# Kernel optimization log

Hardware: AMD Instinct MI355X
Metric: run time of the kernel (lower is better)

Reference implementation:

```python
import jax, jax.numpy as jnp
import numpy as np

DIM = 512; NB = 4; BS = DIM // NB            # EinFFT blocks
DS = 64; DC = 4; EXP = 2; DI = EXP * DIM      # Mamba dims
DTR = DIM // 16                               # dt_rank
BLOCKS = 2; LAM = 0.01; B_SZ = 2; L_SZ = 1024

def layer_norm(x, w, b):
    m = x.mean(-1, keepdims=True)
    v = x.var(-1, keepdims=True)
    return (x - m) / jnp.sqrt(v + 1e-5) * w + b

def softshrink(x, lam):
    return jnp.where(x > lam, x - lam, jnp.where(x < -lam, x + lam, jnp.zeros((), x.dtype)))

def mamba(x, in_proj_w, conv_w, conv_b, x_proj_w, dt_proj_w, dt_proj_b, A_log, D, out_proj_w):
    B, L, _ = x.shape
    xz = x @ in_proj_w.T                      # (B,L,2*DI)
    xm, z = jnp.split(xz, 2, axis=-1)
    # causal depthwise conv1d, keep first L outputs
    xt = xm.transpose(0, 2, 1)                # (B,DI,L)
    conv = jax.lax.conv_general_dilated(xt, conv_w, (1,), [(DC - 1, 0)],
                                        feature_group_count=DI,
                                        dimension_numbers=('NCH', 'OIH', 'NCH'))
    xm = jax.nn.silu((conv + conv_b[None, :, None]).transpose(0, 2, 1))  # (B,L,DI)
    proj = xm @ x_proj_w.T                    # (B,L,DTR+2*DS)
    dt = proj[..., :DTR]
    Bm = proj[..., DTR:DTR + DS]
    Cm = proj[..., DTR + DS:]
    dt = jax.nn.softplus(dt @ dt_proj_w.T + dt_proj_b)   # (B,L,DI)
    A = -jnp.exp(A_log)                       # (DI,DS)

    def step(h, inp):
        dt_t, B_t, C_t, u_t = inp             # (B,DI),(B,DS),(B,DS),(B,DI)
        dA = jnp.exp(dt_t[:, :, None] * A)
        h = dA * h + dt_t[:, :, None] * B_t[:, None, :] * u_t[:, :, None]
        y = jnp.einsum('bds,bs->bd', h, C_t)
        return h, y

    h0 = jnp.zeros((B, DI, DS), x.dtype)
    _, ys = jax.lax.scan(step, h0, (dt.transpose(1, 0, 2), Bm.transpose(1, 0, 2),
                                    Cm.transpose(1, 0, 2), xm.transpose(1, 0, 2)))
    y = ys.transpose(1, 0, 2) + xm * D        # (B,L,DI)
    y = y * jax.nn.silu(z)
    return y @ out_proj_w.T

def einfft(x, cw1, cw2, cb1, cb2):
    B, N, C = x.shape
    xf = jnp.fft.fft2(x.reshape(B, N, NB, BS), axes=(1, 2), norm='ortho')
    mul = lambda t, w: jnp.einsum('BNbd,bdk->BNbk', t, w)
    r1 = jax.nn.relu(mul(xf.real, cw1[0]) - mul(xf.imag, cw1[1]) + cb1[0])
    i1 = jax.nn.relu(mul(xf.real, cw1[1]) + mul(xf.imag, cw1[0]) + cb1[1])
    r2 = softshrink(mul(r1, cw2[0]) - mul(i1, cw2[1]) + cb2[0], LAM)
    i2 = softshrink(mul(r1, cw2[1]) + mul(i1, cw2[0]) + cb2[1], LAM)
    out = jnp.fft.ifft2(r2 + 1j * i2, axes=(1, 2), norm='ortho')
    return out.real.astype(x.dtype).reshape(B, N, C)

def setup_inputs() -> dict:
    key = jax.random.key(0)
    ks = jax.random.split(key, 16)
    r = lambda i, shape, s: jax.random.normal(ks[i], shape, jnp.float32) * s
    A_log = jnp.log(jnp.tile(jnp.arange(1, DS + 1, dtype=jnp.float32), (DI, 1)))
    return {
        'x': jax.random.normal(ks[0], (B_SZ, L_SZ, DIM), jnp.float32),
        'ln_w': jnp.ones((DIM,), jnp.float32), 'ln_b': jnp.zeros((DIM,), jnp.float32),
        'in_proj_w': r(1, (2 * DI, DIM), 0.02),
        'conv_w': r(2, (DI, 1, DC), 0.1), 'conv_b': jnp.zeros((DI,), jnp.float32),
        'x_proj_w': r(3, (DTR + 2 * DS, DI), 0.02),
        'dt_proj_w': r(4, (DI, DTR), 0.02),
        'dt_proj_b': jnp.full((DI,), float(np.log(np.expm1(0.01))), jnp.float32),
        'A_log': A_log, 'D': jnp.ones((DI,), jnp.float32),
        'out_proj_w': r(5, (DIM, DI), 0.02),
        'norm2_w': jnp.ones((DIM,), jnp.float32), 'norm2_b': jnp.zeros((DIM,), jnp.float32),
        'cw1': r(6, (2, NB, BS, BS), 0.02), 'cw2': r(7, (2, NB, BS, BS), 0.02),
        'cb1': r(8, (2, NB, BS), 0.02), 'cb2': r(9, (2, NB, BS), 0.02),
    }

def reference(x, ln_w, ln_b, in_proj_w, conv_w, conv_b, x_proj_w, dt_proj_w, dt_proj_b,
              A_log, D, out_proj_w, norm2_w, norm2_b, cw1, cw2, cb1, cb2):
    for _ in range(BLOCKS):
        x = x + mamba(layer_norm(x, ln_w, ln_b), in_proj_w, conv_w, conv_b,
                      x_proj_w, dt_proj_w, dt_proj_b, A_log, D, out_proj_w)
        x = x + einfft(layer_norm(x, norm2_w, norm2_b), cw1, cw2, cb1, cb2)
    return x
```

## Files before the change

### kernel.cpp

```cpp
#include <hip/hip_runtime.h>

typedef unsigned short u16;
typedef __attribute__((ext_vector_type(8))) short bf8;
typedef __attribute__((ext_vector_type(4))) float f4;

__device__ __forceinline__ float bf2f(u16 b) {
    return __uint_as_float(((unsigned)b) << 16);
}
__device__ __forceinline__ u16 f2bf(float f) {
    unsigned u = __float_as_uint(f);
    u += 0x7fffu + ((u >> 16) & 1u);
    return (u16)(u >> 16);
}
__device__ __forceinline__ void pack8f(const float* v, u16* dst) {
    uint r0 = (uint)f2bf(v[0]) | ((uint)f2bf(v[1]) << 16);
    uint r1 = (uint)f2bf(v[2]) | ((uint)f2bf(v[3]) << 16);
    uint r2 = (uint)f2bf(v[4]) | ((uint)f2bf(v[5]) << 16);
    uint r3 = (uint)f2bf(v[6]) | ((uint)f2bf(v[7]) << 16);
    *(uint4*)dst = make_uint4(r0, r1, r2, r3);
}
__device__ __forceinline__ bf8 neg8(bf8 v) {
    union { bf8 b; uint u[4]; } t; t.b = v;
    t.u[0] ^= 0x80008000u; t.u[1] ^= 0x80008000u;
    t.u[2] ^= 0x80008000u; t.u[3] ^= 0x80008000u;
// ... 106 lines not shown
}

#define LSTR 40
template <int TAF, int EPI>
__global__ __launch_bounds__(256)
void mgemm_k(const void* __restrict__ Ap, const u16* __restrict__ Bp,
             float* __restrict__ D, int N, int K, int lda, int ldb, int ldc,
             long bsA, long bsB, long bsC,
             const float* __restrict__ bias, const float* __restrict__ res) {
    const float* Af = (const float*)Ap + blockIdx.z * bsA;
    const u16*  Ab  = (const u16*)Ap + blockIdx.z * bsA;
    const u16*  B   = Bp + blockIdx.z * bsB;
    D += blockIdx.z * bsC;

    __shared__ u16 As[64 * LSTR];
    __shared__ u16 Bs[64 * LSTR];
    const int tid = threadIdx.x;
    const int lane = tid & 63;
    const int w = tid >> 6, wm = w & 1, wn = w >> 1;
    const int m0 = blockIdx.y * 64, n0 = blockIdx.x * 64;
    const int fr = (lane & 15), fq = (lane >> 4);

    f4 acc[2][2] = {};

    for (int k0 = 0; k0 < K; k0 += 32) {
        {
            const int ar = tid >> 2, aks = (tid & 3) << 3;
            if constexpr (TAF == 1) {
                *(uint4*)&As[ar * LSTR + aks] =
                    *(const uint4*)(Ab + (long)(m0 + ar) * lda + k0 + aks);
            } else if constexpr (TAF == 2) {
                const float* p = Af + (long)(m0 + ar) * lda + k0 + aks;
                float4 x = *(const float4*)p, y = *(const float4*)(p + 4);
#pragma unroll
                for (int pt = 1; pt < 4; ++pt) {
                    const float* pp = p + (long)pt * bsA;
                    float4 x1 = *(const float4*)pp, y1 = *(const float4*)(pp + 4);
                    x.x += x1.x; x.y += x1.y; x.z += x1.z; x.w += x1.w;
                    y.x += y1.x; y.y += y1.y; y.z += y1.z; y.w += y1.w;
                }
                float tv[8];
                tv[0] = x.x; tv[1] = x.y; tv[2] = x.z; tv[3] = x.w;
                tv[4] = y.x; tv[5] = y.y; tv[6] = y.z; tv[7] = y.w;
                pack8f(tv, &As[ar * LSTR + aks]);
            } else {
                const float* p = Af + (long)(m0 + ar) * lda + k0 + aks;
                float tv[8];
                float4 x = *(const float4*)p, y = *(const float4*)(p + 4);
                tv[0] = x.x; tv[1] = x.y; tv[2] = x.z; tv[3] = x.w;
                tv[4] = y.x; tv[5] = y.y; tv[6] = y.z; tv[7] = y.w;
                pack8f(tv, &As[ar * LSTR + aks]);
            }
        }
        {
            const int br = tid >> 2, bks = (tid & 3) << 3;
            uint4 raw = make_uint4(0, 0, 0, 0);
            if (n0 + br < N)
                raw = *(const uint4*)(B + (long)(n0 + br) * ldb + k0 + bks);
            *(uint4*)&Bs[br * LSTR + bks] = raw;
        }
        __syncthreads();
        bf8 af[2], bff[2];
#pragma unroll
        for (int t = 0; t < 2; t++) {
            af[t]  = *(bf8*)&As[(wm * 32 + t * 16 + fr) * LSTR + (fq << 3)];
            bff[t] = *(bf8*)&Bs[(wn * 32 + t * 16 + fr) * LSTR + (fq << 3)];
        }
#pragma unroll
        for (int i = 0; i < 2; i++)
#pragma unroll
            for (int j = 0; j < 2; j++)
                acc[i][j] = __builtin_amdgcn_mfma_f32_16x16x32_bf16(
                    af[i], bff[j], acc[i][j], 0, 0, 0);
        __syncthreads();
    }

#pragma unroll
    for (int i = 0; i < 2; i++) {
#pragma unroll
        for (int j = 0; j < 2; j++) {
            const int gmb = m0 + wm * 32 + i * 16 + (fq << 2);
            const int gn  = n0 + wn * 32 + j * 16 + fr;
            if (gn >= N) continue;
            float v[4];
#pragma unroll
            for (int e = 0; e < 4; e++) v[e] = acc[i][j][e];
            if constexpr (EPI == 1) {
                float bb = bias[gn];
#pragma unroll
                for (int e = 0; e < 4; e++) {
                    float t = v[e] + bb;
                    v[e] = (t > 20.f) ? t : log1pf(__expf(t));
                }
            }
#pragma unroll
            for (int e = 0; e < 4; e++) {
                long idx = (long)(gmb + e) * ldc + gn;
                float t = v[e];
                if constexpr (EPI == 2) t += res[idx];
                D[idx] = t;
            }
        }
    }
}

__global__ __launch_bounds__(256)
void gemm128_k(const u16* __restrict__ A, const u16* __restrict__ B,
               float* __restrict__ D, int K, int lda, int ldb, int ldc) {
    __shared__ u16 As[128 * LSTR];
    __shared__ u16 Bs[128 * LSTR];
    const int tid = threadIdx.x, lane = tid & 63;
    const int w = tid >> 6, wm = w & 1, wn = w >> 1;
    const int m0 = blockIdx.y * 128, n0 = blockIdx.x * 128;
    const int fr = lane & 15, fq = lane >> 4;
    f4 acc[4][4] = {};

    for (int k0 = 0; k0 < K; k0 += 32) {
#pragma unroll
        for (int j = 0; j < 2; ++j) {
            int idx = tid + j * 256;
            int row = idx >> 2, col = (idx & 3) << 3;
            *(uint4*)&As[row * LSTR + col] =
                *(const uint4*)(A + (long)(m0 + row) * lda + k0 + col);
            *(uint4*)&Bs[row * LSTR + col] =
                *(const uint4*)(B + (long)(n0 + row) * ldb + k0 + col);
        }
        __syncthreads();
        bf8 af[4], bfv[4];
#pragma unroll
        for (int i = 0; i < 4; ++i) {
            af[i]  = *(bf8*)&As[(wm * 64 + i * 16 + fr) * LSTR + (fq << 3)];
            bfv[i] = *(bf8*)&Bs[(wn * 64 + i * 16 + fr) * LSTR + (fq << 3)];
        }
#pragma unroll
        for (int i = 0; i < 4; ++i)
#pragma unroll
            for (int j = 0; j < 4; ++j)
                acc[i][j] = __builtin_amdgcn_mfma_f32_16x16x32_bf16(
                    af[i], bfv[j], acc[i][j], 0, 0, 0);
        __syncthreads();
    }
#pragma unroll
    for (int i = 0; i < 4; ++i)
#pragma unroll
        for (int j = 0; j < 4; ++j) {
            const int gm = m0 + wm * 64 + i * 16 + (fq << 2);
            const int gn = n0 + wn * 64 + j * 16 + fr;
#pragma unroll
            for (int e = 0; e < 4; ++e)
                D[(long)(gm + e) * ldc + gn] = acc[i][j][e];
        }
}

__global__ __launch_bounds__(1024)
void ffw_k(const u16* __restrict__ xn, u16* __restrict__ Orb,
           u16* __restrict__ Oib) {
    const int bz = blockIdx.x;
    const int b = bz >> 7, cg = bz & 127;
    const int t = threadIdx.x;
    const int f = t >> 8, tl = t & 255;
    const int c = cg + f * 128;
    __shared__ float re[4224], im[4224], twr[768], twi[768];
    if (t < 768) {
        float s, cc;
        __sincosf((float)t * -6.1359231515425649e-3f, &s, &cc);
        twr[t] = cc; twi[t] = s;
    }
    float* rf = re + f * 1056;
    float* mf = im + f * 1056;
    const u16* src = xn + ((long)b * 1024) * 512 + c;
#pragma unroll
    for (int r = 0; r < 4; ++r) {
        int n = tl + r * 256;
        float v = bf2f(src[(long)n * 512]);
        int a = n + (n >> 5);
        rf[a] = v; mf[a] = 0.f;
    }
    __syncthreads();
#pragma unroll
    for (int st = 0; st < 5; ++st) {
        const int qsh = 8 - 2 * st;
        const int q = 1 << qsh;
        const int len = q << 2;
        const int m = 1 << (2 * st);
        int j = tl & (q - 1);
        int g = tl >> qsh;
        int i0 = g * len + j;
        int a0 = i0 + (i0 >> 5);
        int i1 = i0 + q,     a1 = i1 + (i1 >> 5);
        int i2 = i0 + 2 * q, a2 = i2 + (i2 >> 5);
        int i3 = i0 + 3 * q, a3 = i3 + (i3 >> 5);
        float ar = rf[a0], ai = mf[a0];
        float br = rf[a1], bi = mf[a1];
        float cr = rf[a2], ci = mf[a2];
        float dr = rf[a3], di = mf[a3];
        float t0r = ar + cr, t0i = ai + ci;
        float t1r = ar - cr, t1i = ai - ci;
        float t2r = br + dr, t2i = bi + di;
        float u = br - dr, v = bi - di;
        rf[a0] = t0r + t2r; mf[a0] = t0i + t2i;
        {
            int k = j * m;
            float wr = twr[k], wi = twi[k];
            float xr = t1r + v, xi = t1i - u;
            rf[a1] = xr * wr - xi * wi;
            mf[a1] = xr * wi + xi * wr;
        }
        {
            int k = 2 * j * m;
            float wr = twr[k], wi = twi[k];
            float xr = t0r - t2r, xi = t0i - t2i;
            rf[a2] = xr * wr - xi * wi;
            mf[a2] = xr * wi + xi * wr;
        }
        {
            int k = 3 * j * m;
            float wr = twr[k], wi = twi[k];
            float xr = t1r - v, xi = t1i + u;
            rf[a3] = xr * wr - xi * wi;
            mf[a3] = xr * wi + xi * wr;
        }
        __syncthreads();
    }
    u16* drp = Orb + ((long)(b * 512 + c)) * 1024;
    u16* dip = Oib + ((long)(b * 512 + c)) * 1024;
#pragma unroll
    for (int r = 0; r < 4; ++r) {
        int kf = tl + r * 256;
        int sidx = digrev10(kf);
        int a = sidx + (sidx >> 5);
        float r0 = re[a],        i0v = im[a];
        float r1 = re[1056 + a], i1v = im[1056 + a];
        float r2 = re[2112 + a], i2v = im[2112 + a];
        float r3 = re[3168 + a], i3v = im[3168 + a];
        float vr, vi;
        if (f == 0)      { vr = r0 + r1 + r2 + r3;     vi = i0v + i1v + i2v + i3v; }
        else if (f == 1) { vr = r0 + i1v - r2 - i3v;   vi = i0v - r1 - i2v + r3; }
        else if (f == 2) { vr = r0 - r1 + r2 - r3;     vi = i0v - i1v + i2v - i3v; }
        else             { vr = r0 - i1v - r2 + i3v;   vi = i0v + r1 - i2v - r3; }
        drp[kf] = f2bf(vr * 0.015625f);
        dip[kf] = f2bf(vi * 0.015625f);
    }
}

__global__ __launch_bounds__(1024)
void ifw_k(const u16* __restrict__ X2r, const u16* __restrict__ X2i,
           float* __restrict__ Yc) {
    const int bz = blockIdx.x;
    const int b = bz >> 7, cg = bz & 127;
    const int t = threadIdx.x;
    const int f = t >> 8, tl = t & 255;
    const int c = cg + f * 128;
    __shared__ float re[4224], im[4224], twr[768], twi[768];
    if (t < 768) {
        float s, cc;
        __sincosf((float)t * 6.1359231515425649e-3f, &s, &cc);
        twr[t] = cc; twi[t] = s;
    }
    const u16* sr = X2r + ((long)(b * 512 + c)) * 1024;
    const u16* si = X2i + ((long)(b * 512 + c)) * 1024;
    float* rf = re + f * 1056;
    float* mf = im + f * 1056;
    const int k4 = tl * 4;
    {
        uint2 pr = *(const uint2*)&sr[k4];
        uint2 pi = *(const uint2*)&si[k4];
        u16 rv[4] = {(u16)(pr.x & 0xFFFF), (u16)(pr.x >> 16),
                     (u16)(pr.y & 0xFFFF), (u16)(pr.y >> 16)};
        u16 iv[4] = {(u16)(pi.x & 0xFFFF), (u16)(pi.x >> 16),
                     (u16)(pi.y & 0xFFFF), (u16)(pi.y >> 16)};
#pragma unroll
        for (int e = 0; e < 4; ++e) {
            int idx = k4 + e;
            int a = idx + (idx >> 5);
            rf[a] = bf2f(rv[e]);
            mf[a] = bf2f(iv[e]);
        }
    }
    __syncthreads();
    float vr[4], vi[4];
#pragma unroll
    for (int e = 0; e < 4; ++e) {
        int idx = k4 + e;
        int a = idx + (idx >> 5);
        float r0 = re[a],        i0v = im[a];
        float r1 = re[1056 + a], i1v = im[1056 + a];
        float r2 = re[2112 + a], i2v = im[2112 + a];
        float r3 = re[3168 + a], i3v = im[3168 + a];
        if (f == 0)      { vr[e] = r0 + r1 + r2 + r3;     vi[e] = i0v + i1v + i2v + i3v; }
        else if (f == 1) { vr[e] = r0 - i1v - r2 + i3v;   vi[e] = i0v + r1 - i2v - r3; }
        else if (f == 2) { vr[e] = r0 - r1 + r2 - r3;     vi[e] = i0v - i1v + i2v - i3v; }
        else             { vr[e] = r0 + i1v - r2 - i3v;   vi[e] = i0v - r1 - i2v + r3; }
        vr[e] *= 0.5f; vi[e] *= 0.5f;
    }
    __syncthreads();
#pragma unroll
    for (int e = 0; e < 4; ++e) {
        int idx = k4 + e;
        int a = idx + (idx >> 5);
        rf[a] = vr[e]; mf[a] = vi[e];
    }
    __syncthreads();
#pragma unroll
    for (int st = 0; st < 5; ++st) {
        const int qsh = 8 - 2 * st;
        const int q = 1 << qsh;
        const int len = q << 2;
        const int m = 1 << (2 * st);
        int j = tl & (q - 1);
        int g = tl >> qsh;
        int i0 = g * len + j;
        int a0 = i0 + (i0 >> 5);
        int i1 = i0 + q,     a1 = i1 + (i1 >> 5);
        int i2 = i0 + 2 * q, a2 = i2 + (i2 >> 5);
        int i3 = i0 + 3 * q, a3 = i3 + (i3 >> 5);
        float ar = rf[a0], ai = mf[a0];
        float br = rf[a1], bi = mf[a1];
        float cr = rf[a2], ci = mf[a2];
        float dr = rf[a3], di = mf[a3];
        float t0r = ar + cr, t0i = ai + ci;
        float t1r = ar - cr, t1i = ai - ci;
        float t2r = br + dr, t2i = bi + di;
        float u = br - dr, v = bi - di;
        rf[a0] = t0r + t2r; mf[a0] = t0i + t2i;
        {
            int k = j * m;
            float wr = twr[k], wi = twi[k];
            float xr = t1r - v, xi = t1i + u;
            rf[a1] = xr * wr - xi * wi;
            mf[a1] = xr * wi + xi * wr;
        }
        {
            int k = 2 * j * m;
            float wr = twr[k], wi = twi[k];
            float xr = t0r - t2r, xi = t0i - t2i;
            rf[a2] = xr * wr - xi * wi;
            mf[a2] = xr * wi + xi * wr;
        }
        {
            int k = 3 * j * m;
            float wr = twr[k], wi = twi[k];
            float xr = t1r + v, xi = t1i - u;
            rf[a3] = xr * wr - xi * wi;
            mf[a3] = xr * wi + xi * wr;
        }
        __syncthreads();
    }
    float* d = Yc + ((long)(b * 512 + c)) * 1024;
#pragma unroll
    for (int r = 0; r < 4; ++r) {
        int n = tl + r * 256;
        int sidx = digrev10(n);
        int a = sidx + (sidx >> 5);
        d[n] = rf[a] * 0.03125f;
    }
}

__global__ __launch_bounds__(256)
void transadd_k(float* __restrict__ xbuf, const float* __restrict__ Yc) {
    const int b = blockIdx.z;
    const int c0 = blockIdx.x * 64, n0 = blockIdx.y * 64;
    __shared__ float T[64][65];
    const int tid = threadIdx.x;
    const int r = tid >> 2, q = (tid & 3) * 16;
    const float* src = Yc + ((long)(b * 512 + c0 + r)) * 1024 + n0 + q;
#pragma unroll
    for (int k = 0; k < 4; ++k) {
        float4 v = *(const float4*)(src + k * 4);
        T[r][q + k * 4 + 0] = v.x; T[r][q + k * 4 + 1] = v.y;
        T[r][q + k * 4 + 2] = v.z; T[r][q + k * 4 + 3] = v.w;
    }
    __syncthreads();
    float* dst = xbuf + ((long)(b * 1024 + n0 + r)) * 512 + c0 + q;
#pragma unroll
    for (int k = 0; k < 4; ++k) {
        float4 w = *(const float4*)(dst + k * 4);
        w.x += T[q + k * 4 + 0][r]; w.y += T[q + k * 4 + 1][r];
        w.z += T[q + k * 4 + 2][r]; w.w += T[q + k * 4 + 3][r];
        *(float4*)(dst + k * 4) = w;
    }
}

#define LSTR2 136
template <int ACT>
__global__ __launch_bounds__(256)
void cmix_k(const u16* __restrict__ Xr, const u16* __restrict__ Xi,
            const u16* __restrict__ WT, const float* __restrict__ cb,
            u16* __restrict__ Or, u16* __restrict__ Oi) {
    const int z = blockIdx.z, b = z >> 2, nb = z & 3;
    const u16* Ar = Xr + (long)b * 524288 + nb * 131072;
    const u16* Ai = Xi + (long)b * 524288 + nb * 131072;
    const u16* Wr = WT + nb * 16384;
    const u16* Wi = WT + 65536 + nb * 16384;
    u16* Dr = Or + (long)b * 524288 + nb * 131072;
    u16* Di = Oi + (long)b * 524288 + nb * 131072;
    __shared__ u16 Ars[64 * LSTR2], Ais[64 * LSTR2], Brs[64 * LSTR2], Bis[64 * LSTR2];
    const int tid = threadIdx.x, lane = tid & 63;
    const int w = tid >> 6, wm = w & 1, wn = w >> 1;
    const int m0 = blockIdx.y * 64, n0 = blockIdx.x * 64;
    const int fr = (lane & 15), fq = (lane >> 4);
    f4 accr[2][2] = {}, acci[2][2] = {};

    {
        const int am = tid & 63, akb = (tid >> 6) << 3;
#pragma unroll
        for (int kk = 0; kk < 4; ++kk) {
            const int kb = kk * 32 + akb;
            u16 tr[8], ti[8];
#pragma unroll
            for (int j = 0; j < 8; j++) {
                long off = (long)(kb + j) * 1024 + m0 + am;
                tr[j] = Ar[off]; ti[j] = Ai[off];
            }
            uint r0 = (uint)tr[0] | ((uint)tr[1] << 16);
            uint r1 = (uint)tr[2] | ((uint)tr[3] << 16);
            uint r2 = (uint)tr[4] | ((uint)tr[5] << 16);
            uint r3 = (uint)tr[6] | ((uint)tr[7] << 16);
            *(uint4*)&Ars[am * LSTR2 + kb] = make_uint4(r0, r1, r2, r3);
            r0 = (uint)ti[0] | ((uint)ti[1] << 16);
            r1 = (uint)ti[2] | ((uint)ti[3] << 16);
            r2 = (uint)ti[4] | ((uint)ti[5] << 16);
            r3 = (uint)ti[6] | ((uint)ti[7] << 16);
            *(uint4*)&Ais[am * LSTR2 + kb] = make_uint4(r0, r1, r2, r3);
        }
        const int br = tid >> 2, bks = (tid & 3) << 3;
#pragma unroll
        for (int kk = 0; kk < 4; ++kk) {
            const int kb = kk * 32 + bks;
            *(uint4*)&Brs[br * LSTR2 + kb] =
                *(const uint4*)(Wr + (long)(n0 + br) * 128 + kb);
            *(uint4*)&Bis[br * LSTR2 + kb] =
                *(const uint4*)(Wi + (long)(n0 + br) * 128 + kb);
        }
    }
    __syncthreads();

#pragma unroll
    for (int kq = 0; kq < 4; ++kq) {
        const int kc = kq * 32 + (fq << 3);
        bf8 arf[2], aif[2], brf[2], bif[2];
#pragma unroll
        for (int t = 0; t < 2; t++) {
            arf[t] = *(bf8*)&Ars[(wm * 32 + t * 16 + fr) * LSTR2 + kc];
            aif[t] = *(bf8*)&Ais[(wm * 32 + t * 16 + fr) * LSTR2 + kc];
            brf[t] = *(bf8*)&Brs[(wn * 32 + t * 16 + fr) * LSTR2 + kc];
            bif[t] = *(bf8*)&Bis[(wn * 32 + t * 16 + fr) * LSTR2 + kc];
        }
        bf8 nai[2] = { neg8(aif[0]), neg8(aif[1]) };
#pragma unroll
        for (int i = 0; i < 2; i++)
#pragma unroll
            for (int j = 0; j < 2; j++) {
                accr[i][j] = __builtin_amdgcn_mfma_f32_16x16x32_bf16(arf[i], brf[j], accr[i][j], 0, 0, 0);
                accr[i][j] = __builtin_amdgcn_mfma_f32_16x16x32_bf16(nai[i], bif[j], accr[i][j], 0, 0, 0);
                acci[i][j] = __builtin_amdgcn_mfma_f32_16x16x32_bf16(arf[i], bif[j], acci[i][j], 0, 0, 0);
                acci[i][j] = __builtin_amdgcn_mfma_f32_16x16x32_bf16(aif[i], brf[j], acci[i][j], 0, 0, 0);
            }
    }

#pragma unroll
    for (int i = 0; i < 2; i++)
#pragma unroll
        for (int j = 0; j < 2; j++) {
            const int gmb = m0 + wm * 32 + i * 16 + (fq << 2);
            const int gn  = n0 + wn * 32 + j * 16 + fr;
            const float bbr = cb[nb * 128 + gn];
            const float bbi = cb[512 + nb * 128 + gn];
            u16 pr[4], pi[4];
#pragma unroll
            for (int e = 0; e < 4; e++) {
                float vr = accr[i][j][e] + bbr;
                float vi = acci[i][j][e] + bbi;
                if (ACT == 0) {
                    vr = fmaxf(vr, 0.f);
                    vi = fmaxf(vi, 0.f);
                } else {
                    vr = (vr > 0.01f) ? vr - 0.01f : ((vr < -0.01f) ? vr + 0.01f : 0.f);
                    vi = (vi > 0.01f) ? vi - 0.01f : ((vi < -0.01f) ? vi + 0.01f : 0.f);
                }
                pr[e] = f2bf(vr); pi[e] = f2bf(vi);
            }
            uint2 wr2, wi2;
            wr2.x = (uint)pr[0] | ((uint)pr[1] << 16);
            wr2.y = (uint)pr[2] | ((uint)pr[3] << 16);
            wi2.x = (uint)pi[0] | ((uint)pi[1] << 16);
            wi2.y = (uint)pi[2] | ((uint)pi[3] << 16);
            *(uint2*)&Dr[(long)gn * 1024 + gmb] = wr2;
            *(uint2*)&Di[(long)gn * 1024 + gmb] = wi2;
        }
}

__global__ __launch_bounds__(256)
void conv_k(const float* __restrict__ xz, const float* __restrict__ cw,
            const float* __restrict__ cb, u16* __restrict__ u) {
    int idx = blockIdx.x * 256 + threadIdx.x;
    int d = idx & 1023;
    int l = (idx >> 10) & 1023;
    int b = idx >> 20;
    float acc = cb[d];
    const float* base = xz + (long)b * 1024 * 2048 + d;
#pragma unroll
    for (int j = 0; j < 4; j++) {
        int li = l - 3 + j;
        if (li >= 0) acc = fmaf(cw[d * 4 + j], base[(long)li * 2048], acc);
    }
    float sig = 1.f / (1.f + __expf(-acc));
    u[idx] = f2bf(acc * sig);
}

__global__ __launch_bounds__(256)
void scan1_k(const float* __restrict__ dtL, const u16* __restrict__ uLb,
             const float* __restrict__ Pb, const float* __restrict__ alog,
             u16* __restrict__ Hb, float* __restrict__ Sbuf,
             const int* __restrict__ flag) {
    const int dg = blockIdx.x, c = blockIdx.y, b = blockIdx.z;
    const int tid = threadIdx.x;
    const int d = dg * 256 + tid;
    const int t0 = c * 16;
    __shared__ float Bls[16][64];
    {
        int r = tid >> 4, cg = (tid & 15) << 2;
        const float* src = Pb + ((long)(b * 1024 + t0 + r)) * 160 + 32 + cg;
        float4 v0 = *(const float4*)src;
        float4 v1 = *(const float4*)(src + 327680);
        float4 v2 = *(const float4*)(src + 655360);
        float4 v3 = *(const float4*)(src + 983040);
        v0.x += v1.x + v2.x + v3.x;
        v0.y += v1.y + v2.y + v3.y;
        v0.z += v1.z + v2.z + v3.z;
        v0.w += v1.w + v2.w + v3.w;
        *(float4*)&Bls[r][cg] = v0;
    }
    __syncthreads();

    float h[64];
#pragma unroll
    for (int s = 0; s < 64; s++) h[s] = 0.f;
    float S = 0.f;
    const float* dtp = dtL + (long)(b * 1024 + t0) * 1024 + d;
    const u16* up = uLb + (long)(b * 1024 + t0) * 1024 + d;

    if (flag[1]) {
        for (int t = 0; t < 16; ++t) {
            float dt = dtp[(long)t * 1024];
            float uu = bf2f(up[(long)t * 1024]);
            float dtu = dt * uu;
            S += dt;
            float q = __expf(-dt);
            float q2 = q * q, q3 = q2 * q, q4 = q2 * q2;
            float a0 = q, a1 = q2, a2 = q3, a3 = q4;
            const float4* B4p = (const float4*)&Bls[t][0];
#pragma unroll
            for (int sg = 0; sg < 16; ++sg) {
                float4 B4 = B4p[sg];
                h[sg * 4 + 0] = a0 * h[sg * 4 + 0] + dtu * B4.x;
                h[sg * 4 + 1] = a1 * h[sg * 4 + 1] + dtu * B4.y;
                h[sg * 4 + 2] = a2 * h[sg * 4 + 2] + dtu * B4.z;
                h[sg * 4 + 3] = a3 * h[sg * 4 + 3] + dtu * B4.w;
                a0 *= q4; a1 *= q4; a2 *= q4; a3 *= q4;
            }
        }
    } else {
        float A[64];
        const float* ap = alog + (long)d * 64;
#pragma unroll
        for (int s = 0; s < 64; s += 4) {
            float4 a4 = *(const float4*)(ap + s);
            A[s] = -__expf(a4.x); A[s + 1] = -__expf(a4.y);
            A[s + 2] = -__expf(a4.z); A[s + 3] = -__expf(a4.w);
        }
        for (int t = 0; t < 16; ++t) {
            float dt = dtp[(long)t * 1024];
            float uu = bf2f(up[(long)t * 1024]);
            float dtu = dt * uu;
            S += dt;
            const float4* B4p = (const float4*)&Bls[t][0];
#pragma unroll
            for (int sg = 0; sg < 16; ++sg) {
                float4 B4 = B4p[sg];
                h[sg * 4 + 0] = __expf(dt * A[sg * 4 + 0]) * h[sg * 4 + 0] + dtu * B4.x;
                h[sg * 4 + 1] = __expf(dt * A[sg * 4 + 1]) * h[sg * 4 + 1] + dtu * B4.y;
                h[sg * 4 + 2] = __expf(dt * A[sg * 4 + 2]) * h[sg * 4 + 2] + dtu * B4.z;
                h[sg * 4 + 3] = __expf(dt * A[sg * 4 + 3]) * h[sg * 4 + 3] + dtu * B4.w;
            }
        }
    }
    u16* Hp = Hb + ((((long)(b * 64 + c)) * 1024 + d) << 6);
#pragma unroll
    for (int s = 0; s < 64; s += 4) {
        uint2 p;
        p.x = ((__float_as_uint(h[s]) + 0x8000u) >> 16) |
              ((__float_as_uint(h[s + 1]) + 0x8000u) & 0xFFFF0000u);
        p.y = ((__float_as_uint(h[s + 2]) + 0x8000u) >> 16) |
              ((__float_as_uint(h[s + 3]) + 0x8000u) & 0xFFFF0000u);
        *(uint2*)&Hp[s] = p;
    }
    Sbuf[(b * 64 + c) * 1024 + d] = S;
}

__global__ __launch_bounds__(256)
void scan2_k(const float* __restrict__ alog, const float* __restrict__ Sbuf,
             u16* __restrict__ Hb) {
    int idx = blockIdx.x * 256 + threadIdx.x;
    int s = idx & 63, d = (idx >> 6) & 1023, b = idx >> 16;
    float A = -__expf(alog[(long)d * 64 + s]);
    float carry = 0.f;
    for (int c = 0; c < 64; ++c) {
        float S = Sbuf[(b * 64 + c) * 1024 + d];
        float P = __expf(A * S);
        long off = ((((long)(b * 64 + c)) * 1024 + d) << 6) + s;
        float H = bf2f(Hb[off]);
        Hb[off] = (u16)((__float_as_uint(carry) + 0x8000u) >> 16);
        carry = P * carry + H;
    }
}

__global__ __launch_bounds__(256)
void scan3_k(const float* __restrict__ dtL, const u16* __restrict__ uLb,
             const float* __restrict__ xz, const float* __restrict__ Pb,
             const float* __restrict__ alog, const u16* __restrict__ Hb,
             const float* __restrict__ Dw, const int* __restrict__ flag,
             u16* __restrict__ y2) {
    const int dg = blockIdx.x, c = blockIdx.y, b = blockIdx.z;
    const int tid = threadIdx.x;
    const int d = dg * 256 + tid;
    const int t0 = c * 16;
    __shared__ float Bls[16][64];
    __shared__ float Cls[16][64];
    {
        int r = tid >> 4, cg = (tid & 15) << 2;
        const float* src = Pb + ((long)(b * 1024 + t0 + r)) * 160 + 32 + cg;
        float4 v0 = *(const float4*)src;
        float4 v1 = *(const float4*)(src + 327680);
        float4 v2 = *(const float4*)(src + 655360);
        float4 v3 = *(const float4*)(src + 983040);
        v0.x += v1.x + v2.x + v3.x;
        v0.y += v1.y + v2.y + v3.y;
        v0.z += v1.z + v2.z + v3.z;
        v0.w += v1.w + v2.w + v3.w;
        *(float4*)&Bls[r][cg] = v0;
        float4 c0 = *(const float4*)(src + 64);
        float4 c1 = *(const float4*)(src + 64 + 327680);
        float4 c2 = *(const float4*)(src + 64 + 655360);
        float4 c3 = *(const float4*)(src + 64 + 983040);
        c0.x += c1.x + c2.x + c3.x;
        c0.y += c1.y + c2.y + c3.y;
        c0.z += c1.z + c2.z + c3.z;
        c0.w += c1.w + c2.w + c3.w;
        *(float4*)&Cls[r][cg] = c0;
    }
    __syncthreads();

    float h[64];
    const u16* Hp = Hb + ((((long)(b * 64 + c)) * 1024 + d) << 6);
#pragma unroll
    for (int s = 0; s < 64; s += 4) {
        uint2 p = *(const uint2*)&Hp[s];
        h[s]     = __uint_as_float(p.x << 16);
        h[s + 1] = __uint_as_float(p.x & 0xFFFF0000u);
        h[s + 2] = __uint_as_float(p.y << 16);
        h[s + 3] = __uint_as_float(p.y & 0xFFFF0000u);
    }
    const float Dd = Dw[d];
    const float* dtp = dtL + (long)(b * 1024 + t0) * 1024 + d;
    const u16* up = uLb + (long)(b * 1024 + t0) * 1024 + d;
    const float* zp = xz + (long)(b * 1024 + t0) * 2048 + 1024 + d;
    u16* y2p = y2 + (long)(b * 1024 + t0) * 1024 + d;

    if (flag[1]) {
        for (int t = 0; t < 16; ++t) {
            float dt = dtp[(long)t * 1024];
            float uu = bf2f(up[(long)t * 1024]);
            float zz = zp[(long)t * 2048];
            float dtu = dt * uu;
            float y = 0.f;
            float q = __expf(-dt);
            float q2 = q * q, q3 = q2 * q, q4 = q2 * q2;
            float a0 = q, a1 = q2, a2 = q3, a3 = q4;
            const float4* B4p = (const float4*)&Bls[t][0];
            const float4* C4p = (const float4*)&Cls[t][0];
#pragma unroll
            for (int sg = 0; sg < 16; ++sg) {
                float4 B4 = B4p[sg];
                float4 C4 = C4p[sg];
                h[sg * 4 + 0] = a0 * h[sg * 4 + 0] + dtu * B4.x;
                y = fmaf(h[sg * 4 + 0], C4.x, y);
                h[sg * 4 + 1] = a1 * h[sg * 4 + 1] + dtu * B4.y;
                y = fmaf(h[sg * 4 + 1], C4.y, y);
                h[sg * 4 + 2] = a2 * h[sg * 4 + 2] + dtu * B4.z;
                y = fmaf(h[sg * 4 + 2], C4.z, y);
                h[sg * 4 + 3] = a3 * h[sg * 4 + 3] + dtu * B4.w;
                y = fmaf(h[sg * 4 + 3], C4.w, y);
                a0 *= q4; a1 *= q4; a2 *= q4; a3 *= q4;
            }
            float g = zz / (1.f + __expf(-zz));
            y2p[(long)t * 1024] = f2bf((y + uu * Dd) * g);
        }
    } else {
        float A[64];
        const float* ap = alog + (long)d * 64;
#pragma unroll
        for (int s = 0; s < 64; s += 4) {
            float4 a4 = *(const float4*)(ap + s);
            A[s] = -__expf(a4.x); A[s + 1] = -__expf(a4.y);
            A[s + 2] = -__expf(a4.z); A[s + 3] = -__expf(a4.w);
        }
        for (int t = 0; t < 16; ++t) {
            float dt = dtp[(long)t * 1024];
            float uu = bf2f(up[(long)t * 1024]);
            float zz = zp[(long)t * 2048];
            float dtu = dt * uu;
            float y = 0.f;
            const float4* B4p = (const float4*)&Bls[t][0];
            const float4* C4p = (const float4*)&Cls[t][0];
#pragma unroll
            for (int sg = 0; sg < 16; ++sg) {
                float4 B4 = B4p[sg];
                float4 C4 = C4p[sg];
                h[sg * 4 + 0] = __expf(dt * A[sg * 4 + 0]) * h[sg * 4 + 0] + dtu * B4.x;
                y = fmaf(h[sg * 4 + 0], C4.x, y);
                h[sg * 4 + 1] = __expf(dt * A[sg * 4 + 1]) * h[sg * 4 + 1] + dtu * B4.y;
                y = fmaf(h[sg * 4 + 1], C4.y, y);
                h[sg * 4 + 2] = __expf(dt * A[sg * 4 + 2]) * h[sg * 4 + 2] + dtu * B4.z;
                y = fmaf(h[sg * 4 + 2], C4.z, y);
                h[sg * 4 + 3] = __expf(dt * A[sg * 4 + 3]) * h[sg * 4 + 3] + dtu * B4.w;
                y = fmaf(h[sg * 4 + 3], C4.w, y);
            }
            float g = zz / (1.f + __expf(-zz));
            y2p[(long)t * 1024] = f2bf((y + uu * Dd) * g);
        }
    }
}

extern "C" void kernel_launch(void* const* d_in, const int* in_sizes, int n_in,
                              void* d_out, int out_size, void* d_ws, size_t ws_size,
                              hipStream_t stream) {
    float* ws = (float*)d_ws;
    int* flag = (int*)ws;
    size_t o = 64;
    float* xbuf  = ws + o; o += 1048576;
    float* xz    = ws + o; o += 4194304;
    float* dtL   = ws + o; o += 2097152;
    u16* xnb     = (u16*)(ws + o); o += 524288;
    u16* wInpB   = (u16*)(ws + o); o += 524288;
    u16* wXpB    = (u16*)(ws + o); o += 81920;
    u16* wDtB    = (u16*)(ws + o); o += 16384;
    u16* wOutB   = (u16*)(ws + o); o += 262144;
    u16* WT1     = (u16*)(ws + o); o += 65536;
    u16* WT2     = (u16*)(ws + o); o += 65536;
    float* wConv = ws + o; o += 4096;
    float* wAlog = ws + o; o += 65536;
    float* wLnW  = ws + o; o += 512;
    float* wLnB  = ws + o; o += 512;
    float* wConvB= ws + o; o += 1024;
    float* wDtBias=ws + o; o += 1024;
    float* wD    = ws + o; o += 1024;
    float* wN2w  = ws + o; o += 512;
    float* wN2b  = ws + o; o += 512;
    float* wCb1  = ws + o; o += 1024;
    float* wCb2  = ws + o; o += 1024;
    float* Hreg  = ws + o; o += 4194304;
    float* Sbuf  = ws + o; o += 131072;
    float* Pbuf2 = ws + o; o += 1310720;
    u16* uLb     = (u16*)(ws + o); o += 1048576;
    u16* y2b     = (u16*)(ws + o); o += 524288;
    u16* Hb    = (u16*)Hreg;
    float* Yc  = dtL;
    u16* xzb  = (u16*)xz;
    u16* Xrb  = xzb;
    u16* Xib  = xzb + 1048576;
    u16* r1b  = xzb + 2097152;
    u16* i1b  = xzb + 3145728;
    u16* X2rb = xzb + 4194304;
    u16* X2ib = xzb + 5242880;

    dim3 blk(256);

    detect_k<<<1, 1, 0, stream>>>((const u16*)d_in[8], flag);

    CvtArgs ca;
    void* dsts[18] = {xbuf, wLnW, wLnB, wInpB, wConv, wConvB, wXpB, wDtB, wDtBias,
                      wAlog, wD, wOutB, wN2w, wN2b, WT1, WT2, wCb1, wCb2};
    int obf[18]    = {0,    0,    0,    1,     0,     0,      1,    1,    0,
                      0,     0,  1,     0,    0,    2,   2,   0,    0};
    for (int i = 0; i < 18; i++) {
        ca.src[i] = d_in[i];
        ca.dst[i] = dsts[i];
        ca.n[i] = in_sizes[i];
        ca.obf[i] = obf[i];
    }
    cvt_all_k<<<dim3(64, 18), blk, 0, stream>>>(ca, flag);
    achk_k<<<256, blk, 0, stream>>>(wAlog, flag);

    for (int it = 0; it < 2; ++it) {
        ln_k<<<2048, blk, 0, stream>>>(xbuf, wLnW, wLnB, xnb);
        gemm128_k<<<dim3(16, 16), blk, 0, stream>>>(
            xnb, wInpB, xz, 512, 512, 512, 2048);
        conv_k<<<8192, blk, 0, stream>>>(xz, wConv, wConvB, uLb);
        mgemm_k<1, 0><<<dim3(3, 32, 4), blk, 0, stream>>>(
            uLb, wXpB, Pbuf2, 160, 256, 1024, 1024, 160,
            256, 256, 327680, nullptr, nullptr);
        mgemm_k<2, 1><<<dim3(16, 32, 1), blk, 0, stream>>>(
            Pbuf2, wDtB, dtL, 1024, 32, 160, 32, 1024, 327680, 0, 0, wDtBias, nullptr);
        scan1_k<<<dim3(4, 64, 2), blk, 0, stream>>>(dtL, uLb, Pbuf2, wAlog, Hb, Sbuf, flag);
        scan2_k<<<512, blk, 0, stream>>>(wAlog, Sbuf, Hb);
        scan3_k<<<dim3(4, 64, 2), blk, 0, stream>>>(dtL, uLb, xz, Pbuf2, wAlog, Hb, wD, flag, y2b);
        mgemm_k<1, 2><<<dim3(8, 32, 1), blk, 0, stream>>>(
            y2b, wOutB, xbuf, 512, 1024, 1024, 1024, 512, 0, 0, 0, nullptr, xbuf);

        ln_k<<<2048, blk, 0, stream>>>(xbuf, wN2w, wN2b, xnb);
        ffw_k<<<256, dim3(1024), 0, stream>>>(xnb, Xrb, Xib);
        cmix_k<0><<<dim3(2, 16, 8), blk, 0, stream>>>(Xrb, Xib, WT1, wCb1, r1b, i1b);
        cmix_k<1><<<dim3(2, 16, 8), blk, 0, stream>>>(r1b, i1b, WT2, wCb2, X2rb, X2ib);
        ifw_k<<<256, dim3(1024), 0, stream>>>(X2rb, X2ib, Yc);
        transadd_k<<<dim3(8, 16, 2), blk, 0, stream>>>(xbuf, Yc);
    }

    out_k<<<(out_size + 255) / 256, blk, 0, stream>>>(xbuf, d_out, out_size, flag);
}
```

Before: 445.8 us.

## Split FFT into per-channel kernels plus combine passes; halve scan state per thread

The fused 1024-thread FFT kernels, which did the length-4 block DFT through shared memory, are split into 256-thread per-channel FFT kernels. Separate elementwise kernels now do the 4-point combine, with fp32 intermediates in new workspace buffers. This adds global traffic and two launches in exchange for smaller blocks and more of them. The scan1/scan3 kernels now split the 64 state entries across two threads per channel, with a shuffle reduction for y, to cut register pressure and double the thread count. scan2 gains software prefetch of the next chunk's values.

```diff
diff --git a/kernel.cpp b/kernel.cpp
--- a/kernel.cpp
+++ b/kernel.cpp
@@ -282,22 +282,18 @@
         }
 }
 
-__global__ __launch_bounds__(1024)
-void ffw_k(const u16* __restrict__ xn, u16* __restrict__ Orb,
-           u16* __restrict__ Oib) {
+__global__ __launch_bounds__(256)
+void fftc_k(const u16* __restrict__ xn, float* __restrict__ Pr,
+            float* __restrict__ Pi) {
     const int bz = blockIdx.x;
-    const int b = bz >> 7, cg = bz & 127;
-    const int t = threadIdx.x;
-    const int f = t >> 8, tl = t & 255;
-    const int c = cg + f * 128;
-    __shared__ float re[4224], im[4224], twr[768], twi[768];
-    if (t < 768) {
+    const int b = bz >> 9, c = bz & 511;
+    const int tl = threadIdx.x;
+    __shared__ float rf[1056], mf[1056], twr[768], twi[768];
+    for (int i = tl; i < 768; i += 256) {
         float s, cc;
-        __sincosf((float)t * -6.1359231515425649e-3f, &s, &cc);
-        twr[t] = cc; twi[t] = s;
-    }
-    float* rf = re + f * 1056;
-    float* mf = im + f * 1056;
+        __sincosf((float)i * -6.1359231515425649e-3f, &s, &cc);
+        twr[i] = cc; twi[i] = s;
+    }
     const u16* src = xn + ((long)b * 1024) * 512 + c;
 #pragma unroll
     for (int r = 0; r < 4; ++r) {
@@ -352,83 +348,127 @@
         }
         __syncthreads();
     }
-    u16* drp = Orb + ((long)(b * 512 + c)) * 1024;
-    u16* dip = Oib + ((long)(b * 512 + c)) * 1024;
+    float* drp = Pr + ((long)(b * 512 + c)) * 1024;
+    float* dip = Pi + ((long)(b * 512 + c)) * 1024;
 #pragma unroll
     for (int r = 0; r < 4; ++r) {
         int kf = tl + r * 256;
         int sidx = digrev10(kf);
         int a = sidx + (sidx >> 5);
-        float r0 = re[a],        i0v = im[a];
-        float r1 = re[1056 + a], i1v = im[1056 + a];
-        float r2 = re[2112 + a], i2v = im[2112 + a];
-        float r3 = re[3168 + a], i3v = im[3168 + a];
-        float vr, vi;
-        if (f == 0)      { vr = r0 + r1 + r2 + r3;     vi = i0v + i1v + i2v + i3v; }
-        else if (f == 1) { vr = r0 + i1v - r2 - i3v;   vi = i0v - r1 - i2v + r3; }
-        else if (f == 2) { vr = r0 - r1 + r2 - r3;     vi = i0v - i1v + i2v - i3v; }
-        else             { vr = r0 - i1v - r2 + i3v;   vi = i0v + r1 - i2v - r3; }
-        drp[kf] = f2bf(vr * 0.015625f);
-        dip[kf] = f2bf(vi * 0.015625f);
-    }
-}
-
-__global__ __launch_bounds__(1024)
-void ifw_k(const u16* __restrict__ X2r, const u16* __restrict__ X2i,
-           float* __restrict__ Yc) {
+        drp[kf] = rf[a] * 0.015625f;
+        dip[kf] = mf[a] * 0.015625f;
+    }
+}
+
+__global__ __launch_bounds__(256)
+void comb4_k(const float* __restrict__ Pr, const float* __restrict__ Pi,
+             u16* __restrict__ Xr, u16* __restrict__ Xi) {
+    int idx = blockIdx.x * 256 + threadIdx.x;
+    int n0 = (idx & 255) << 2;
+    int j  = (idx >> 8) & 127;
+    int b  = idx >> 15;
+    const long sb = (long)b * 524288 + (long)j * 1024 + n0;
+    float4 r0 = *(const float4*)&Pr[sb];
+    float4 r1 = *(const float4*)&Pr[sb + 131072];
+    float4 r2 = *(const float4*)&Pr[sb + 262144];
+    float4 r3 = *(const float4*)&Pr[sb + 393216];
+    float4 i0 = *(const float4*)&Pi[sb];
+    float4 i1 = *(const float4*)&Pi[sb + 131072];
+    float4 i2 = *(const float4*)&Pi[sb + 262144];
+    float4 i3 = *(const float4*)&Pi[sb + 393216];
+    float R0[4] = {r0.x, r0.y, r0.z, r0.w}, R1[4] = {r1.x, r1.y, r1.z, r1.w};
+    float R2[4] = {r2.x, r2.y, r2.z, r2.w}, R3[4] = {r3.x, r3.y, r3.z, r3.w};
+    float I0[4] = {i0.x, i0.y, i0.z, i0.w}, I1[4] = {i1.x, i1.y, i1.z, i1.w};
+    float I2[4] = {i2.x, i2.y, i2.z, i2.w}, I3[4] = {i3.x, i3.y, i3.z, i3.w};
+    u16 vr[4][4], vi[4][4];
+#pragma unroll
+    for (int e = 0; e < 4; ++e) {
+        vr[0][e] = f2bf(R0[e] + R1[e] + R2[e] + R3[e]);
+        vi[0][e] = f2bf(I0[e] + I1[e] + I2[e] + I3[e]);
+        vr[1][e] = f2bf(R0[e] + I1[e] - R2[e] - I3[e]);
+        vi[1][e] = f2bf(I0[e] - R1[e] - I2[e] + R3[e]);
+        vr[2][e] = f2bf(R0[e] - R1[e] + R2[e] - R3[e]);
+        vi[2][e] = f2bf(I0[e] - I1[e] + I2[e] - I3[e]);
+        vr[3][e] = f2bf(R0[e] - I1[e] - R2[e] + I3[e]);
+        vi[3][e] = f2bf(I0[e] + R1[e] - I2[e] - R3[e]);
+    }
+#pragma unroll
+    for (int nb = 0; nb < 4; ++nb) {
+        uint2 pr, pi;
+        pr.x = (uint)vr[nb][0] | ((uint)vr[nb][1] << 16);
+        pr.y = (uint)vr[nb][2] | ((uint)vr[nb][3] << 16);
+        pi.x = (uint)vi[nb][0] | ((uint)vi[nb][1] << 16);
+        pi.y = (uint)vi[nb][2] | ((uint)vi[nb][3] << 16);
+        *(uint2*)&Xr[sb + (long)nb * 131072] = pr;
+        *(uint2*)&Xi[sb + (long)nb * 131072] = pi;
+    }
+}
+
+__global__ __launch_bounds__(256)
+void icomb4_k(const u16* __restrict__ X2r, const u16* __restrict__ X2i,
+              float* __restrict__ Cr, float* __restrict__ Ci) {
+    int idx = blockIdx.x * 256 + threadIdx.x;
+    int n0 = (idx & 255) << 2;
+    int j  = (idx >> 8) & 127;
+    int b  = idx >> 15;
+    const long sb = (long)b * 524288 + (long)j * 1024 + n0;
+    float R[4][4], I[4][4];
+#pragma unroll
+    for (int p = 0; p < 4; ++p) {
+        uint2 pr = *(const uint2*)&X2r[sb + (long)p * 131072];
+        uint2 pi = *(const uint2*)&X2i[sb + (long)p * 131072];
+        R[p][0] = bf2f((u16)(pr.x & 0xFFFF)); R[p][1] = bf2f((u16)(pr.x >> 16));
+        R[p][2] = bf2f((u16)(pr.y & 0xFFFF)); R[p][3] = bf2f((u16)(pr.y >> 16));
+        I[p][0] = bf2f((u16)(pi.x & 0xFFFF)); I[p][1] = bf2f((u16)(pi.x >> 16));
+        I[p][2] = bf2f((u16)(pi.y & 0xFFFF)); I[p][3] = bf2f((u16)(pi.y >> 16));
+    }
+    float vr[4][4], vi[4][4];
+#pragma unroll
+    for (int e = 0; e < 4; ++e) {
+        vr[0][e] = (R[0][e] + R[1][e] + R[2][e] + R[3][e]) * 0.5f;
+        vi[0][e] = (I[0][e] + I[1][e] + I[2][e] + I[3][e]) * 0.5f;
+        vr[1][e] = (R[0][e] - I[1][e] - R[2][e] + I[3][e]) * 0.5f;
+        vi[1][e] = (I[0][e] + R[1][e] - I[2][e] - R[3][e]) * 0.5f;
+        vr[2][e] = (R[0][e] - R[1][e] + R[2][e] - R[3][e]) * 0.5f;
+        vi[2][e] = (I[0][e] - I[1][e] + I[2][e] - I[3][e]) * 0.5f;
+        vr[3][e] = (R[0][e] + I[1][e] - R[2][e] - I[3][e]) * 0.5f;
+        vi[3][e] = (I[0][e] - R[1][e] - I[2][e] + R[3][e]) * 0.5f;
+    }
+#pragma unroll
+    for (int nb = 0; nb < 4; ++nb) {
+        *(float4*)&Cr[sb + (long)nb * 131072] =
+            make_float4(vr[nb][0], vr[nb][1], vr[nb][2], vr[nb][3]);
+        *(float4*)&Ci[sb + (long)nb * 131072] =
+            make_float4(vi[nb][0], vi[nb][1], vi[nb][2], vi[nb][3]);
+    }
+}
+
+__global__ __launch_bounds__(256)
+void ifftc_k(const float* __restrict__ Cr, const float* __restrict__ Ci,
+             float* __restrict__ Yc) {
     const int bz = blockIdx.x;
-    const int b = bz >> 7, cg = bz & 127;
-    const int t = threadIdx.x;
-    const int f = t >> 8, tl = t & 255;
-    const int c = cg + f * 128;
-    __shared__ float re[4224], im[4224], twr[768], twi[768];
-    if (t < 768) {
+    const int b = bz >> 9, c = bz & 511;
+    const int tl = threadIdx.x;
+    __shared__ float rf[1056], mf[1056], twr[768], twi[768];
+    for (int i = tl; i < 768; i += 256) {
         float s, cc;
-        __sincosf((float)t * 6.1359231515425649e-3f, &s, &cc);
-        twr[t] = cc; twi[t] = s;
-    }
-    const u16* sr = X2r + ((long)(b * 512 + c)) * 1024;
-    const u16* si = X2i + ((long)(b * 512 + c)) * 1024;
-    float* rf = re + f * 1056;
-    float* mf = im + f * 1056;
+        __sincosf((float)i * 6.1359231515425649e-3f, &s, &cc);
+        twr[i] = cc; twi[i] = s;
+    }
+    const float* sr = Cr + ((long)(b * 512 + c)) * 1024;
+    const float* si = Ci + ((long)(b * 512 + c)) * 1024;
     const int k4 = tl * 4;
     {
-        uint2 pr = *(const uint2*)&sr[k4];
-        uint2 pi = *(const uint2*)&si[k4];
-        u16 rv[4] = {(u16)(pr.x & 0xFFFF), (u16)(pr.x >> 16),
-                     (u16)(pr.y & 0xFFFF), (u16)(pr.y >> 16)};
-        u16 iv[4] = {(u16)(pi.x & 0xFFFF), (u16)(pi.x >> 16),
-                     (u16)(pi.y & 0xFFFF), (u16)(pi.y >> 16)};
+        float4 fr4 = *(const float4*)&sr[k4];
+        float4 fi4 = *(const float4*)&si[k4];
+        float fr[4] = {fr4.x, fr4.y, fr4.z, fr4.w};
+        float fi[4] = {fi4.x, fi4.y, fi4.z, fi4.w};
 #pragma unroll
         for (int e = 0; e < 4; ++e) {
             int idx = k4 + e;
             int a = idx + (idx >> 5);
-            rf[a] = bf2f(rv[e]);
-            mf[a] = bf2f(iv[e]);
-        }
-    }
-    __syncthreads();
-    float vr[4], vi[4];
-#pragma unroll
-    for (int e = 0; e < 4; ++e) {
-        int idx = k4 + e;
-        int a = idx + (idx >> 5);
-        float r0 = re[a],        i0v = im[a];
-        float r1 = re[1056 + a], i1v = im[1056 + a];
-        float r2 = re[2112 + a], i2v = im[2112 + a];
-        float r3 = re[3168 + a], i3v = im[3168 + a];
-        if (f == 0)      { vr[e] = r0 + r1 + r2 + r3;     vi[e] = i0v + i1v + i2v + i3v; }
-        else if (f == 1) { vr[e] = r0 - i1v - r2 + i3v;   vi[e] = i0v + r1 - i2v - r3; }
-        else if (f == 2) { vr[e] = r0 - r1 + r2 - r3;     vi[e] = i0v - i1v + i2v - i3v; }
-        else             { vr[e] = r0 + i1v - r2 - i3v;   vi[e] = i0v - r1 - i2v + r3; }
-        vr[e] *= 0.5f; vi[e] *= 0.5f;
-    }
-    __syncthreads();
-#pragma unroll
-    for (int e = 0; e < 4; ++e) {
-        int idx = k4 + e;
-        int a = idx + (idx >> 5);
-        rf[a] = vr[e]; mf[a] = vi[e];
+            rf[a] = fr[e]; mf[a] = fi[e];
+        }
     }
     __syncthreads();
 #pragma unroll
@@ -645,7 +685,8 @@
              const int* __restrict__ flag) {
     const int dg = blockIdx.x, c = blockIdx.y, b = blockIdx.z;
     const int tid = threadIdx.x;
-    const int d = dg * 256 + tid;
+    const int d = dg * 128 + (tid >> 1);
+    const int sh = tid & 1;
     const int t0 = c * 16;
     __shared__ float Bls[16][64];
     {
@@ -663,9 +704,9 @@
     }
     __syncthreads();
 
-    float h[64];
-#pragma unroll
-    for (int s = 0; s < 64; s++) h[s] = 0.f;
+    float h[32];
+#pragma unroll
+    for (int s = 0; s < 32; s++) h[s] = 0.f;
     float S = 0.f;
     const float* dtp = dtL + (long)(b * 1024 + t0) * 1024 + d;
     const u16* up = uLb + (long)(b * 1024 + t0) * 1024 + d;
@@ -678,10 +719,12 @@
             S += dt;
             float q = __expf(-dt);
             float q2 = q * q, q3 = q2 * q, q4 = q2 * q2;
-            float a0 = q, a1 = q2, a2 = q3, a3 = q4;
-            const float4* B4p = (const float4*)&Bls[t][0];
-#pragma unroll
-            for (int sg = 0; sg < 16; ++sg) {
+            float q8 = q4 * q4, q16 = q8 * q8, q32 = q16 * q16;
+            float qs = sh ? q32 : 1.f;
+            float a0 = q * qs, a1 = q2 * qs, a2 = q3 * qs, a3 = q4 * qs;
+            const float4* B4p = (const float4*)&Bls[t][sh * 32];
+#pragma unroll
+            for (int sg = 0; sg < 8; ++sg) {
                 float4 B4 = B4p[sg];
                 h[sg * 4 + 0] = a0 * h[sg * 4 + 0] + dtu * B4.x;
                 h[sg * 4 + 1] = a1 * h[sg * 4 + 1] + dtu * B4.y;
@@ -691,10 +734,10 @@
             }
         }
     } else {
-        float A[64];
-        const float* ap = alog + (long)d * 64;
-#pragma unroll
-        for (int s = 0; s < 64; s += 4) {
+        float A[32];
+        const float* ap = alog + (long)d * 64 + sh * 32;
+#pragma unroll
+        for (int s = 0; s < 32; s += 4) {
             float4 a4 = *(const float4*)(ap + s);
             A[s] = -__expf(a4.x); A[s + 1] = -__expf(a4.y);
             A[s + 2] = -__expf(a4.z); A[s + 3] = -__expf(a4.w);
@@ -704,9 +747,9 @@
             float uu = bf2f(up[(long)t * 1024]);
             float dtu = dt * uu;
             S += dt;
-            const float4* B4p = (const float4*)&Bls[t][0];
-#pragma unroll
-            for (int sg = 0; sg < 16; ++sg) {
+            const float4* B4p = (const float4*)&Bls[t][sh * 32];
+#pragma unroll
+            for (int sg = 0; sg < 8; ++sg) {
                 float4 B4 = B4p[sg];
                 h[sg * 4 + 0] = __expf(dt * A[sg * 4 + 0]) * h[sg * 4 + 0] + dtu * B4.x;
                 h[sg * 4 + 1] = __expf(dt * A[sg * 4 + 1]) * h[sg * 4 + 1] + dtu * B4.y;
@@ -715,9 +758,9 @@
             }
         }
     }
-    u16* Hp = Hb + ((((long)(b * 64 + c)) * 1024 + d) << 6);
-#pragma unroll
-    for (int s = 0; s < 64; s += 4) {
+    u16* Hp = Hb + ((((long)(b * 64 + c)) * 1024 + d) << 6) + sh * 32;
+#pragma unroll
+    for (int s = 0; s < 32; s += 4) {
         uint2 p;
         p.x = ((__float_as_uint(h[s]) + 0x8000u) >> 16) |
               ((__float_as_uint(h[s + 1]) + 0x8000u) & 0xFFFF0000u);
@@ -725,7 +768,7 @@
               ((__float_as_uint(h[s + 3]) + 0x8000u) & 0xFFFF0000u);
         *(uint2*)&Hp[s] = p;
     }
-    Sbuf[(b * 64 + c) * 1024 + d] = S;
+    if (!sh) Sbuf[(b * 64 + c) * 1024 + d] = S;
 }
 
 __global__ __launch_bounds__(256)
@@ -735,13 +778,21 @@
     int s = idx & 63, d = (idx >> 6) & 1023, b = idx >> 16;
     float A = -__expf(alog[(long)d * 64 + s]);
     float carry = 0.f;
+    long off = ((((long)(b * 64)) * 1024 + d) << 6) + s;
+    int sb = (b * 64) * 1024 + d;
+    float Scur = Sbuf[sb];
+    float Hcur = bf2f(Hb[off]);
     for (int c = 0; c < 64; ++c) {
-        float S = Sbuf[(b * 64 + c) * 1024 + d];
-        float P = __expf(A * S);
-        long off = ((((long)(b * 64 + c)) * 1024 + d) << 6) + s;
-        float H = bf2f(Hb[off]);
+        float Snxt = 0.f, Hnxt = 0.f;
+        if (c < 63) {
+            Snxt = Sbuf[sb + 1024];
+            Hnxt = bf2f(Hb[off + 65536]);
+        }
+        float P = __expf(A * Scur);
         Hb[off] = (u16)((__float_as_uint(carry) + 0x8000u) >> 16);
-        carry = P * carry + H;
+        carry = P * carry + Hcur;
+        Scur = Snxt; Hcur = Hnxt;
+        off += 65536; sb += 1024;
     }
 }
 
@@ -753,7 +804,8 @@
              u16* __restrict__ y2) {
     const int dg = blockIdx.x, c = blockIdx.y, b = blockIdx.z;
     const int tid = threadIdx.x;
-    const int d = dg * 256 + tid;
+    const int d = dg * 128 + (tid >> 1);
+    const int sh = tid & 1;
     const int t0 = c * 16;
     __shared__ float Bls[16][64];
     __shared__ float Cls[16][64];
@@ -781,10 +833,10 @@
     }
     __syncthreads();
 
-    float h[64];
-    const u16* Hp = Hb + ((((long)(b * 64 + c)) * 1024 + d) << 6);
-#pragma unroll
-    for (int s = 0; s < 64; s += 4) {
+    float h[32];
+    const u16* Hp = Hb + ((((long)(b * 64 + c)) * 1024 + d) << 6) + sh * 32;
+#pragma unroll
+    for (int s = 0; s < 32; s += 4) {
         uint2 p = *(const uint2*)&Hp[s];
         h[s]     = __uint_as_float(p.x << 16);
         h[s + 1] = __uint_as_float(p.x & 0xFFFF0000u);
@@ -806,11 +858,13 @@
             float y = 0.f;
             float q = __expf(-dt);
             float q2 = q * q, q3 = q2 * q, q4 = q2 * q2;
-            float a0 = q, a1 = q2, a2 = q3, a3 = q4;
-            const float4* B4p = (const float4*)&Bls[t][0];
-            const float4* C4p = (const float4*)&Cls[t][0];
-#pragma unroll
-            for (int sg = 0; sg < 16; ++sg) {
+            float q8 = q4 * q4, q16 = q8 * q8, q32 = q16 * q16;
+            float qs = sh ? q32 : 1.f;
+            float a0 = q * qs, a1 = q2 * qs, a2 = q3 * qs, a3 = q4 * qs;
+            const float4* B4p = (const float4*)&Bls[t][sh * 32];
+            const float4* C4p = (const float4*)&Cls[t][sh * 32];
+#pragma unroll
+            for (int sg = 0; sg < 8; ++sg) {
                 float4 B4 = B4p[sg];
                 float4 C4 = C4p[sg];
                 h[sg * 4 + 0] = a0 * h[sg * 4 + 0] + dtu * B4.x;
@@ -823,14 +877,17 @@
                 y = fmaf(h[sg * 4 + 3], C4.w, y);
                 a0 *= q4; a1 *= q4; a2 *= q4; a3 *= q4;
             }
-            float g = zz / (1.f + __expf(-zz));
-            y2p[(long)t * 1024] = f2bf((y + uu * Dd) * g);
+            y += __shfl_xor(y, 1);
+            if (!sh) {
+                float g = zz / (1.f + __expf(-zz));
+                y2p[(long)t * 1024] = f2bf((y + uu * Dd) * g);
+            }
         }
     } else {
-        float A[64];
-        const float* ap = alog + (long)d * 64;
-#pragma unroll
-        for (int s = 0; s < 64; s += 4) {
+        float A[32];
+        const float* ap = alog + (long)d * 64 + sh * 32;
+#pragma unroll
+        for (int s = 0; s < 32; s += 4) {
             float4 a4 = *(const float4*)(ap + s);
             A[s] = -__expf(a4.x); A[s + 1] = -__expf(a4.y);
             A[s + 2] = -__expf(a4.z); A[s + 3] = -__expf(a4.w);
@@ -841,10 +898,10 @@
             float zz = zp[(long)t * 2048];
             float dtu = dt * uu;
             float y = 0.f;
-            const float4* B4p = (const float4*)&Bls[t][0];
-            const float4* C4p = (const float4*)&Cls[t][0];
-#pragma unroll
-            for (int sg = 0; sg < 16; ++sg) {
+            const float4* B4p = (const float4*)&Bls[t][sh * 32];
+            const float4* C4p = (const float4*)&Cls[t][sh * 32];
+#pragma unroll
+            for (int sg = 0; sg < 8; ++sg) {
                 float4 B4 = B4p[sg];
                 float4 C4 = C4p[sg];
                 h[sg * 4 + 0] = __expf(dt * A[sg * 4 + 0]) * h[sg * 4 + 0] + dtu * B4.x;
@@ -856,8 +913,11 @@
                 h[sg * 4 + 3] = __expf(dt * A[sg * 4 + 3]) * h[sg * 4 + 3] + dtu * B4.w;
                 y = fmaf(h[sg * 4 + 3], C4.w, y);
             }
-            float g = zz / (1.f + __expf(-zz));
-            y2p[(long)t * 1024] = f2bf((y + uu * Dd) * g);
+            y += __shfl_xor(y, 1);
+            if (!sh) {
+                float g = zz / (1.f + __expf(-zz));
+                y2p[(long)t * 1024] = f2bf((y + uu * Dd) * g);
+            }
         }
     }
 }
@@ -894,6 +954,8 @@
     float* Pbuf2 = ws + o; o += 1310720;
     u16* uLb     = (u16*)(ws + o); o += 1048576;
     u16* y2b     = (u16*)(ws + o); o += 524288;
+    float* Fr    = ws + o; o += 1048576;
+    float* Fi    = ws + o; o += 1048576;
     u16* Hb    = (u16*)Hreg;
     float* Yc  = dtL;
     u16* xzb  = (u16*)xz;
@@ -932,17 +994,19 @@
             256, 256, 327680, nullptr, nullptr);
         mgemm_k<2, 1><<<dim3(16, 32, 1), blk, 0, stream>>>(
             Pbuf2, wDtB, dtL, 1024, 32, 160, 32, 1024, 327680, 0, 0, wDtBias, nullptr);
-        scan1_k<<<dim3(4, 64, 2), blk, 0, stream>>>(dtL, uLb, Pbuf2, wAlog, Hb, Sbuf, flag);
+        scan1_k<<<dim3(8, 64, 2), blk, 0, stream>>>(dtL, uLb, Pbuf2, wAlog, Hb, Sbuf, flag);
         scan2_k<<<512, blk, 0, stream>>>(wAlog, Sbuf, Hb);
-        scan3_k<<<dim3(4, 64, 2), blk, 0, stream>>>(dtL, uLb, xz, Pbuf2, wAlog, Hb, wD, flag, y2b);
+        scan3_k<<<dim3(8, 64, 2), blk, 0, stream>>>(dtL, uLb, xz, Pbuf2, wAlog, Hb, wD, flag, y2b);
         mgemm_k<1, 2><<<dim3(8, 32, 1), blk, 0, stream>>>(
             y2b, wOutB, xbuf, 512, 1024, 1024, 1024, 512, 0, 0, 0, nullptr, xbuf);
 
         ln_k<<<2048, blk, 0, stream>>>(xbuf, wN2w, wN2b, xnb);
-        ffw_k<<<256, dim3(1024), 0, stream>>>(xnb, Xrb, Xib);
+        fftc_k<<<1024, blk, 0, stream>>>(xnb, Fr, Fi);
+        comb4_k<<<256, blk, 0, stream>>>(Fr, Fi, Xrb, Xib);
         cmix_k<0><<<dim3(2, 16, 8), blk, 0, stream>>>(Xrb, Xib, WT1, wCb1, r1b, i1b);
         cmix_k<1><<<dim3(2, 16, 8), blk, 0, stream>>>(r1b, i1b, WT2, wCb2, X2rb, X2ib);
-        ifw_k<<<256, dim3(1024), 0, stream>>>(X2rb, X2ib, Yc);
+        icomb4_k<<<256, blk, 0, stream>>>(X2rb, X2ib, Fr, Fi);
+        ifftc_k<<<1024, blk, 0, stream>>>(Fr, Fi, Yc);
         transadd_k<<<dim3(8, 16, 2), blk, 0, stream>>>(xbuf, Yc);
     }
 
```

Result: slower. 478.4 us (+7.3%).
